# Performance work log

Hardware: AMD Instinct MI355X
Metric: run time of the kernel (lower is better)

## Reference

```python
import jax, jax.numpy as jnp
import numpy as np

N_NODES = 50000
N_EDGES = 800000
IN_DIM = 5
HID = (32, 64, 128, 64, 32)
OUT_DIM = 2
EPS = 1e-5  # nn.BatchNorm1d default eps


def _bn(x, g, b):
    # BatchNorm1d in training mode: batch (biased) statistics over nodes
    m = jnp.mean(x, axis=0)
    v = jnp.var(x, axis=0)
    return (x - m) * jax.lax.rsqrt(v + EPS) * g + b


def setup_inputs() -> dict:
    key = jax.random.key(0)
    ks = jax.random.split(key, 40)
    it = iter(range(40))
    def nrm(shape, s=0.1):
        return jax.random.normal(ks[next(it)], shape, jnp.float32) * s
    inp = {}
    inp["x"] = jax.random.normal(ks[next(it)], (N_NODES, IN_DIM), jnp.float32)
    inp["edge_index"] = jax.random.randint(ks[next(it)], (2, N_EDGES), 0, N_NODES, jnp.int32)
    # input embedding: Linear(5,32) -> ReLU -> BatchNorm1d(32)
    inp["emb_W"] = nrm((IN_DIM, HID[0]))
    inp["emb_b"] = jnp.zeros((HID[0],), jnp.float32)
    inp["emb_g"] = jnp.ones((HID[0],), jnp.float32)
    inp["emb_beta"] = jnp.zeros((HID[0],), jnp.float32)
    # 4 GraphConv blocks
    for i in range(len(HID) - 1):
        din, dout = HID[i], HID[i + 1]
        inp[f"b{i}_Wrel"] = nrm((din, dout))   # lin_rel weight (has bias)
        inp[f"b{i}_brel"] = jnp.zeros((dout,), jnp.float32)
        inp[f"b{i}_Wroot"] = nrm((din, dout))  # lin_root weight (no bias)
        inp[f"b{i}_g"] = jnp.ones((dout,), jnp.float32)
        inp[f"b{i}_beta"] = jnp.zeros((dout,), jnp.float32)
    # output MLP: Linear(32,16) -> ReLU -> Linear(16,2)
    inp["out_W1"] = nrm((HID[-1], HID[-1] // 2))
    inp["out_b1"] = jnp.zeros((HID[-1] // 2,), jnp.float32)
    inp["out_W2"] = nrm((HID[-1] // 2, OUT_DIM))
    inp["out_b2"] = jnp.zeros((OUT_DIM,), jnp.float32)
    return inp


def reference(x, edge_index,
              emb_W, emb_b, emb_g, emb_beta,
              b0_Wrel, b0_brel, b0_Wroot, b0_g, b0_beta,
              b1_Wrel, b1_brel, b1_Wroot, b1_g, b1_beta,
              b2_Wrel, b2_brel, b2_Wroot, b2_g, b2_beta,
              b3_Wrel, b3_brel, b3_Wroot, b3_g, b3_beta,
              out_W1, out_b1, out_W2, out_b2):
    src, dst = edge_index[0], edge_index[1]
    # input embedding: Linear -> ReLU -> BN
    h = jnp.maximum(x @ emb_W + emb_b, 0.0)
    h = _bn(h, emb_g, emb_beta)
    blocks = [
        (b0_Wrel, b0_brel, b0_Wroot, b0_g, b0_beta),
        (b1_Wrel, b1_brel, b1_Wroot, b1_g, b1_beta),
        (b2_Wrel, b2_brel, b2_Wroot, b2_g, b2_beta),
        (b3_Wrel, b3_brel, b3_Wroot, b3_g, b3_beta),
    ]
    for Wrel, brel, Wroot, g, beta in blocks:
        # GraphConv (aggr='add'): lin_rel(sum_{j in N(i)} x_j) + lin_root(x_i)
        agg = jax.ops.segment_sum(h[src], dst, num_segments=N_NODES)
        h = agg @ Wrel + brel + h @ Wroot
        # BN then ReLU (GNNBlock order)
        h = jnp.maximum(_bn(h, g, beta), 0.0)
    # output MLP
    h = jnp.maximum(h @ out_W1 + out_b1, 0.0)
    return h @ out_W2 + out_b2
```

## Files before the change

### kernel.cpp

```cpp
#include <hip/hip_runtime.h>

#define N_NODES 50000
#define N_EDGES 800000
#define BN_EPS 1e-5f

typedef unsigned int   u32;
typedef unsigned short u16;

__device__ __forceinline__ void fma4(float4& a, float s, const float4& w) {
    a.x += s * w.x; a.y += s * w.y; a.z += s * w.z; a.w += s * w.w;
}
__device__ __forceinline__ void add4(float4& a, const float4& b) {
    a.x += b.x; a.y += b.y; a.z += b.z; a.w += b.w;
}
__device__ __forceinline__ u16 f2bf(float f) {
    union { u32 i; float f; } c; c.f = f;
    return (u16)((c.i + 0x7FFFu + ((c.i >> 16) & 1u)) >> 16);
}
__device__ __forceinline__ float4 bf4(uint2 w) {
    union { u32 i; float f; } a, b, c, d;
    a.i = w.x << 16; b.i = w.x & 0xFFFF0000u;
    c.i = w.y << 16; d.i = w.y & 0xFFFF0000u;
    return make_float4(a.f, b.f, c.f, d.f);
}
__device__ __forceinline__ uint2 pack4(const float4& v) {
    uint2 w;
    w.x = (u32)f2bf(v.x) | ((u32)f2bf(v.y) << 16);
    w.y = (u32)f2bf(v.z) | ((u32)f2bf(v.w) << 16);
    return w;
}

template <int NY>
__device__ __forceinline__ bool xcd_decode(int nx, int& x, int& y) {
    const int s = blockIdx.x & (8 * NY - 1);
    const int g = blockIdx.x / (8 * NY);
    x = g * 8 + (s & 7);
    y = s >> 3;
    return x < nx;
}
static inline int xcd_grid(int nx, int ny) { return ((nx + 7) / 8 * 8) * ny; }

__global__ void zero_i(int* __restrict__ p, int n) {
    int i = blockIdx.x * blockDim.x + threadIdx.x;
    int stride = gridDim.x * blockDim.x;
    for (; i < n; i += stride) p[i] = 0;
}

__global__ void hist_kernel(const int* __restrict__ dst, int* __restrict__ cnt) {
    int i = blockIdx.x * blockDim.x + threadIdx.x;
    int stride = gridDim.x * blockDim.x;
    for (; i < N_EDGES; i += stride) atomicAdd(&cnt[dst[i]], 1);
}
__global__ void scan1_kernel(const int* __restrict__ cnt, int* __restrict__ rp,
                             int* __restrict__ bsum) {
    __shared__ int s[256];
    int t = threadIdx.x;
    int idx = blockIdx.x * 256 + t;
    int v = (idx < N_NODES) ? cnt[idx] : 0;
    s[t] = v;
    __syncthreads();
    for (int off = 1; off < 256; off <<= 1) {
        int x = 0;
        if (t >= off) x = s[t - off];
        __syncthreads();
        s[t] += x;
        __syncthreads();
    }
    if (idx < N_NODES) rp[idx] = s[t] - v;
    if (t == 255) bsum[blockIdx.x] = s[255];
}
__global__ void scan2_kernel(int* __restrict__ bsum, int nb, float* __restrict__ stats) {
    __shared__ int s[256];
    int t = threadIdx.x;
    for (int i = t; i < 5 * 256; i += 256) stats[i] = 0.f;
    int v = (t < nb) ? bsum[t] : 0;
    s[t] = v;
    __syncthreads();
    for (int off = 1; off < 256; off <<= 1) {
        int x = 0;
        if (t >= off) x = s[t - off];
        __syncthreads();
        s[t] += x;
        __syncthreads();
    }
    if (t < nb) bsum[t] = s[t] - v;
}
__global__ void scan3_kernel(int* __restrict__ rp, const int* __restrict__ bsum,
                             int* __restrict__ cnt) {
    int idx = blockIdx.x * 256 + threadIdx.x;
    if (idx < N_NODES) {
        rp[idx] += bsum[blockIdx.x];
        cnt[idx] = 0;
    }
    if (idx == 0) rp[N_NODES] = N_EDGES;
}
__global__ void fill_kernel(const int* __restrict__ src, const int* __restrict__ dst,
                            const int* __restrict__ rp, int* __restrict__ cur,
                            u16* __restrict__ ssrc) {
    int i = blockIdx.x * blockDim.x + threadIdx.x;
    int stride = gridDim.x * blockDim.x;
    for (; i < N_EDGES; i += stride) {
        int d = dst[i];
        int p = rp[d] + atomicAdd(&cur[d], 1);
        ssrc[p] = (u16)src[i];
    }
}

__global__ __launch_bounds__(256) void emb_fused(
    const float* __restrict__ x, const float* __restrict__ W,
    const float* __restrict__ b, float* __restrict__ out,
    u16* __restrict__ out16, float* __restrict__ stats) {
    __shared__ float lsum[32], lssq[32];
    if (threadIdx.x < 32) { lsum[threadIdx.x] = 0.f; lssq[threadIdx.x] = 0.f; }
    __syncthreads();
    const int o = threadIdx.x & 31;
    const int total = N_NODES * 32;
    float mys = 0.f, myq = 0.f;
    for (int base = blockIdx.x * 256; base < total; base += gridDim.x * 256) {
        int idx = base + threadIdx.x;
        float acc = 0.f;
        if (idx < total) {
            int n = idx >> 5;
            const float* xr = x + n * 5;
            acc = b[o];
#pragma unroll
            for (int k = 0; k < 5; ++k) acc += xr[k] * W[k * 32 + o];
            acc = fmaxf(acc, 0.f);
            out[idx] = acc;
            out16[idx] = f2bf(acc);
        }
        mys += acc;
        myq += acc * acc;
    }
    mys += __shfl_xor(mys, 32);
    myq += __shfl_xor(myq, 32);
    if ((threadIdx.x & 63) < 32) { atomicAdd(&lsum[o], mys); atomicAdd(&lssq[o], myq); }
    __syncthreads();
    if (threadIdx.x < 32) {
        atomicAdd(&stats[threadIdx.x], lsum[threadIdx.x]);
        atomicAdd(&stats[32 + threadIdx.x], lssq[threadIdx.x]);
    }
}

template <int D>
__device__ __forceinline__ void bn_finalize_lds(
    const float* __restrict__ stats, const float* __restrict__ g,
    const float* __restrict__ beta, float* sc, float* sh) {
    const float invN = 1.f / (float)N_NODES;
    for (int f = threadIdx.x; f < D; f += 256) {
        float m = stats[f] * invN;
        float var = stats[D + f] * invN - m * m;
        float a = g[f] * rsqrtf(var + BN_EPS);
        sc[f] = a;
        sh[f] = beta[f] - m * a;
    }
    __syncthreads();
}

__global__ __launch_bounds__(256) void bn_apply16(
    float4* __restrict__ h, u16* __restrict__ out16,
    const float* __restrict__ g, const float* __restrict__ beta,
    const float* __restrict__ stats, int logD) {
    const int D = 1 << logD;
    const int total4 = N_NODES << (logD - 2);
    const float invN = 1.f / (float)N_NODES;
    int idx = blockIdx.x * blockDim.x + threadIdx.x;
    int stride = gridDim.x * blockDim.x;
    for (; idx < total4; idx += stride) {
        int f = (idx & ((D >> 2) - 1)) << 2;
        float4 v = h[idx];
        float* vp = (float*)&v;
#pragma unroll
        for (int c = 0; c < 4; ++c) {
            float m = stats[f + c] * invN;
            float var = stats[D + f + c] * invN - m * m;
            vp[c] = fmaxf((vp[c] - m) * rsqrtf(var + BN_EPS) * g[f + c] + beta[f + c], 0.f);
        }
        h[idx] = v;
        ((uint2*)out16)[idx] = pack4(v);
    }
}

template <int LOGD>
__global__ __launch_bounds__(256) void gather_agg_bf16(
    const u16* __restrict__ h16, const int* __restrict__ rp,
    const u16* __restrict__ ssrc, float4* __restrict__ agg) {
    constexpr int QSH = LOGD - 2;
    int tid = blockIdx.x * 256 + threadIdx.x;
    int node = tid >> QSH;
    if (node >= N_NODES) return;
    int q = tid & ((1 << QSH) - 1);
    int e0 = rp[node], e1 = rp[node + 1];
    float4 acc = make_float4(0.f, 0.f, 0.f, 0.f);
    int e = e0;
    for (; e + 4 <= e1; e += 4) {
        int s0 = ssrc[e], s1 = ssrc[e + 1], s2 = ssrc[e + 2], s3 = ssrc[e + 3];
        uint2 w0 = ((const uint2*)(h16 + ((size_t)s0 << LOGD)))[q];
        uint2 w1 = ((const uint2*)(h16 + ((size_t)s1 << LOGD)))[q];
        uint2 w2 = ((const uint2*)(h16 + ((size_t)s2 << LOGD)))[q];
        uint2 w3 = ((const uint2*)(h16 + ((size_t)s3 << LOGD)))[q];
        float4 v0 = bf4(w0), v1 = bf4(w1), v2 = bf4(w2), v3 = bf4(w3);
        add4(v0, v1); add4(v2, v3); add4(acc, v0); add4(acc, v2);
    }
    for (; e < e1; ++e) {
        float4 v = bf4(((const uint2*)(h16 + ((size_t)ssrc[e] << LOGD)))[q]);
        add4(acc, v);
    }
    agg[tid] = acc;
}

template <int DIN, int DOUT, int OBL>
__global__ __launch_bounds__(256) void gconv_bn0(
    const float* __restrict__ h, const float* __restrict__ agg,
    const float* __restrict__ Wrel, const float* __restrict__ brel,
    const float* __restrict__ Wroot, float* __restrict__ out,
    const float* __restrict__ stats_in, const float* __restrict__ g_in,
    const float* __restrict__ beta_in, const int* __restrict__ deg,
    float* __restrict__ stats_out, int nx) {
    constexpr int NY = 2;
    constexpr int LPN = OBL / 4;
    constexpr int SLOTS = 256 / LPN;
    constexpr int NPT = 4;
    constexpr int KS = 8;
    constexpr int TOT4 = DIN * OBL / 4;
    int bx, by;
    if (!xcd_decode<NY>(nx, bx, by)) return;
    __shared__ __align__(16) float wl[2 * DIN * OBL];
    __shared__ __align__(16) float sc[DIN];
    __shared__ __align__(16) float sh[DIN];
    __shared__ float lsum[OBL], lssq[OBL];
    const int ob0 = by * OBL;
    for (int e4 = threadIdx.x; e4 < TOT4; e4 += 256) {
        int k = e4 / (OBL / 4);
        int j = (e4 % (OBL / 4)) * 4;
        ((float4*)wl)[e4] = *(const float4*)(Wrel + (size_t)k * DOUT + ob0 + j);
        ((float4*)wl)[TOT4 + e4] = *(const float4*)(Wroot + (size_t)k * DOUT + ob0 + j);
    }
    if (threadIdx.x < OBL) { lsum[threadIdx.x] = 0.f; lssq[threadIdx.x] = 0.f; }
    bn_finalize_lds<DIN>(stats_in, g_in, beta_in, sc, sh);

    const int q = threadIdx.x & (LPN - 1);
    const int slot = threadIdx.x / LPN;
    const int o0 = ob0 + q * 4;
    const int nbase = bx * (SLOTS * NPT) + slot;

    float degf[NPT];
#pragma unroll
    for (int i = 0; i < NPT; ++i) {
        int n = nbase + i * SLOTS;
        degf[i] = (n < N_NODES) ? (float)deg[n] : 0.f;
    }

    float4 bias = *(const float4*)(brel + o0);
    float4 acc[NPT];
#pragma unroll
    for (int i = 0; i < NPT; ++i) acc[i] = bias;

#pragma unroll 1
    for (int s = 0; s < DIN / KS; ++s) {
        const int k0 = s * KS;
        float4 s2[2] = {((const float4*)sc)[k0 / 4], ((const float4*)sc)[k0 / 4 + 1]};
        float4 t2[2] = {((const float4*)sh)[k0 / 4], ((const float4*)sh)[k0 / 4 + 1]};
        const float* scp = (const float*)s2;
        const float* shp = (const float*)t2;
        float4 hv[NPT][2], av[NPT][2];
#pragma unroll
        for (int i = 0; i < NPT; ++i) {
            int n = nbase + i * SLOTS;
            int nn = (n < N_NODES) ? n : 0;
            const float4* hr = (const float4*)(h + (size_t)nn * DIN + k0);
            const float4* ar = (const float4*)(agg + (size_t)nn * DIN + k0);
            hv[i][0] = hr[0]; hv[i][1] = hr[1];
            av[i][0] = ar[0]; av[i][1] = ar[1];
        }
#pragma unroll
        for (int kk = 0; kk < KS; ++kk) {
            float4 wr = *(const float4*)&wl[(k0 + kk) * OBL + q * 4];
            float4 wo = *(const float4*)&wl[DIN * OBL + (k0 + kk) * OBL + q * 4];
#pragma unroll
            for (int i = 0; i < NPT; ++i) {
                float a  = fmaf(((const float*)av[i])[kk], scp[kk], degf[i] * shp[kk]);
                float hh = fmaf(((const float*)hv[i])[kk], scp[kk], shp[kk]);
                fma4(acc[i], a, wr);
                fma4(acc[i], hh, wo);
            }
        }
    }
#pragma unroll
    for (int i = 0; i < NPT; ++i) {
        int n = nbase + i * SLOTS;
        if (n < N_NODES)
            *(float4*)(out + (size_t)n * DOUT + o0) = acc[i];
        else
            acc[i] = make_float4(0.f, 0.f, 0.f, 0.f);
    }
    float4 s4 = make_float4(0.f, 0.f, 0.f, 0.f);
    float4 q4 = make_float4(0.f, 0.f, 0.f, 0.f);
#pragma unroll
    for (int i = 0; i < NPT; ++i) {
        s4.x += acc[i].x; s4.y += acc[i].y; s4.z += acc[i].z; s4.w += acc[i].w;
        q4.x += acc[i].x * acc[i].x; q4.y += acc[i].y * acc[i].y;
        q4.z += acc[i].z * acc[i].z; q4.w += acc[i].w * acc[i].w;
    }
#pragma unroll
    for (int d = LPN; d < 64; d <<= 1) {
        s4.x += __shfl_xor(s4.x, d); s4.y += __shfl_xor(s4.y, d);
        s4.z += __shfl_xor(s4.z, d); s4.w += __shfl_xor(s4.w, d);
        q4.x += __shfl_xor(q4.x, d); q4.y += __shfl_xor(q4.y, d);
        q4.z += __shfl_xor(q4.z, d); q4.w += __shfl_xor(q4.w, d);
    }
    if ((threadIdx.x & 63) < LPN) {
        int c = q * 4;
        atomicAdd(&lsum[c + 0], s4.x); atomicAdd(&lsum[c + 1], s4.y);
        atomicAdd(&lsum[c + 2], s4.z); atomicAdd(&lsum[c + 3], s4.w);
        atomicAdd(&lssq[c + 0], q4.x); atomicAdd(&lssq[c + 1], q4.y);
        atomicAdd(&lssq[c + 2], q4.z); atomicAdd(&lssq[c + 3], q4.w);
    }
    __syncthreads();
    if (threadIdx.x < OBL) {
        atomicAdd(&stats_out[ob0 + threadIdx.x], lsum[threadIdx.x]);
        atomicAdd(&stats_out[DOUT + ob0 + threadIdx.x], lssq[threadIdx.x]);
    }
}

template <int DIN, int DOUT, int OBL>
__global__ __launch_bounds__(256) void gconv_lds(
    const float* __restrict__ h, const float* __restrict__ agg,
    const float* __restrict__ Wrel, const float* __restrict__ brel,
    const float* __restrict__ Wroot, float* __restrict__ out,
    float* __restrict__ stats_out, int nx) {
    constexpr int NY = DOUT / OBL;
    constexpr int LPN = OBL / 4;
    constexpr int SLOTS = 256 / LPN;
    constexpr int NPT = 4;
    constexpr int KS = 8;
    constexpr int TOT4 = DIN * OBL / 4;
    int bx, by;
    if (!xcd_decode<NY>(nx, bx, by)) return;
    __shared__ __align__(16) float wl[2 * DIN * OBL];
    __shared__ float lsum[OBL], lssq[OBL];
    const int ob0 = by * OBL;
    for (int e4 = threadIdx.x; e4 < TOT4; e4 += 256) {
        int k = e4 / (OBL / 4);
        int j = (e4 % (OBL / 4)) * 4;
        ((float4*)wl)[e4] = *(const float4*)(Wrel + (size_t)k * DOUT + ob0 + j);
        ((float4*)wl)[TOT4 + e4] = *(const float4*)(Wroot + (size_t)k * DOUT + ob0 + j);
    }
    if (threadIdx.x < OBL) { lsum[threadIdx.x] = 0.f; lssq[threadIdx.x] = 0.f; }
    __syncthreads();

    const int q = threadIdx.x & (LPN - 1);
    const int slot = threadIdx.x / LPN;
    const int o0 = ob0 + q * 4;
    const int nbase = bx * (SLOTS * NPT) + slot;

    float4 bias = *(const float4*)(brel + o0);
    float4 acc[NPT];
#pragma unroll
    for (int i = 0; i < NPT; ++i) acc[i] = bias;

#pragma unroll 1
    for (int s = 0; s < DIN / KS; ++s) {
        const int k0 = s * KS;
        float4 hv[NPT][2], av[NPT][2];
#pragma unroll
        for (int i = 0; i < NPT; ++i) {
            int n = nbase + i * SLOTS;
            int nn = (n < N_NODES) ? n : 0;
            const float4* hr = (const float4*)(h + (size_t)nn * DIN + k0);
            const float4* ar = (const float4*)(agg + (size_t)nn * DIN + k0);
            hv[i][0] = hr[0]; hv[i][1] = hr[1];
            av[i][0] = ar[0]; av[i][1] = ar[1];
        }
#pragma unroll
        for (int kk = 0; kk < KS; ++kk) {
            float4 wr = *(const float4*)&wl[(k0 + kk) * OBL + q * 4];
            float4 wo = *(const float4*)&wl[DIN * OBL + (k0 + kk) * OBL + q * 4];
#pragma unroll
            for (int i = 0; i < NPT; ++i) {
                fma4(acc[i], ((const float*)av[i])[kk], wr);
                fma4(acc[i], ((const float*)hv[i])[kk], wo);
            }
        }
    }
#pragma unroll
    for (int i = 0; i < NPT; ++i) {
        int n = nbase + i * SLOTS;
        if (n < N_NODES)
            *(float4*)(out + (size_t)n * DOUT + o0) = acc[i];
        else
            acc[i] = make_float4(0.f, 0.f, 0.f, 0.f);
    }
    float4 s4 = make_float4(0.f, 0.f, 0.f, 0.f);
    float4 q4 = make_float4(0.f, 0.f, 0.f, 0.f);
#pragma unroll
    for (int i = 0; i < NPT; ++i) {
        s4.x += acc[i].x; s4.y += acc[i].y; s4.z += acc[i].z; s4.w += acc[i].w;
        q4.x += acc[i].x * acc[i].x; q4.y += acc[i].y * acc[i].y;
        q4.z += acc[i].z * acc[i].z; q4.w += acc[i].w * acc[i].w;
    }
#pragma unroll
    for (int d = LPN; d < 64; d <<= 1) {
        s4.x += __shfl_xor(s4.x, d); s4.y += __shfl_xor(s4.y, d);
        s4.z += __shfl_xor(s4.z, d); s4.w += __shfl_xor(s4.w, d);
        q4.x += __shfl_xor(q4.x, d); q4.y += __shfl_xor(q4.y, d);
        q4.z += __shfl_xor(q4.z, d); q4.w += __shfl_xor(q4.w, d);
    }
    if ((threadIdx.x & 63) < LPN) {
        int c = q * 4;
        atomicAdd(&lsum[c + 0], s4.x); atomicAdd(&lsum[c + 1], s4.y);
        atomicAdd(&lsum[c + 2], s4.z); atomicAdd(&lsum[c + 3], s4.w);
        atomicAdd(&lssq[c + 0], q4.x); atomicAdd(&lssq[c + 1], q4.y);
        atomicAdd(&lssq[c + 2], q4.z); atomicAdd(&lssq[c + 3], q4.w);
    }
    __syncthreads();
    if (threadIdx.x < OBL) {
        atomicAdd(&stats_out[ob0 + threadIdx.x], lsum[threadIdx.x]);
        atomicAdd(&stats_out[DOUT + ob0 + threadIdx.x], lssq[threadIdx.x]);
    }
}

template <int DIN, int DOUT, int OBL>
__global__ __launch_bounds__(256) void prem_bn(
    const float* __restrict__ h, const float* __restrict__ Wrel,
    const float* __restrict__ brel, const float* __restrict__ Wroot,
    u16* __restrict__ P16, float* __restrict__ Q,
    const float* __restrict__ stats_in, const float* __restrict__ g_in,
    const float* __restrict__ beta_in, int nx) {
    constexpr int NY = DOUT / OBL;
    constexpr int LPN = OBL / 4;
    constexpr int SLOTS = 256 / LPN;
    constexpr int NPT = 4;
    constexpr int KS = 8;
    constexpr int TOT4 = DIN * OBL / 4;
    int bx, by;
    if (!xcd_decode<NY>(nx, bx, by)) return;
    __shared__ __align__(16) float wl[2 * DIN * OBL];
    __shared__ __align__(16) float sc[DIN];
    __shared__ __align__(16) float sh[DIN];
    const int ob0 = by * OBL;
    for (int e4 = threadIdx.x; e4 < TOT4; e4 += 256) {
        int k = e4 / (OBL / 4);
        int j = (e4 % (OBL / 4)) * 4;
        ((float4*)wl)[e4] = *(const float4*)(Wrel + (size_t)k * DOUT + ob0 + j);
        ((float4*)wl)[TOT4 + e4] = *(const float4*)(Wroot + (size_t)k * DOUT + ob0 + j);
    }
    bn_finalize_lds<DIN>(stats_in, g_in, beta_in, sc, sh);

    const int q = threadIdx.x & (LPN - 1);
    const int slot = threadIdx.x / LPN;
    const int o0 = ob0 + q * 4;
    const int nbase = bx * (SLOTS * NPT) + slot;

    float4 bias = *(const float4*)(brel + o0);
    float4 accp[NPT], accq[NPT];
#pragma unroll
    for (int i = 0; i < NPT; ++i) {
        accp[i] = make_float4(0.f, 0.f, 0.f, 0.f);
        accq[i] = bias;
    }

#pragma unroll 1
    for (int s = 0; s < DIN / KS; ++s) {
        const int k0 = s * KS;
        float4 s2[2] = {((const float4*)sc)[k0 / 4], ((const float4*)sc)[k0 / 4 + 1]};
        float4 t2[2] = {((const float4*)sh)[k0 / 4], ((const float4*)sh)[k0 / 4 + 1]};
        const float* scp = (const float*)s2;
        const float* shp = (const float*)t2;
        float4 hv[NPT][2];
#pragma unroll
        for (int i = 0; i < NPT; ++i) {
            int n = nbase + i * SLOTS;
            int nn = (n < N_NODES) ? n : 0;
            const float4* hr = (const float4*)(h + (size_t)nn * DIN + k0);
            hv[i][0] = hr[0]; hv[i][1] = hr[1];
        }
#pragma unroll
        for (int kk = 0; kk < KS; ++kk) {
            float4 wr = *(const float4*)&wl[(k0 + kk) * OBL + q * 4];
            float4 wo = *(const float4*)&wl[DIN * OBL + (k0 + kk) * OBL + q * 4];
#pragma unroll
            for (int i = 0; i < NPT; ++i) {
                float hh = fmaxf(fmaf(((const float*)hv[i])[kk], scp[kk], shp[kk]), 0.f);
                fma4(accp[i], hh, wr);
                fma4(accq[i], hh, wo);
            }
        }
    }
#pragma unroll
    for (int i = 0; i < NPT; ++i) {
        int n = nbase + i * SLOTS;
        if (n < N_NODES) {
            *(uint2*)(P16 + (size_t)n * DOUT + o0) = pack4(accp[i]);
            *(float4*)(Q + (size_t)n * DOUT + o0) = accq[i];
        }
    }
}

template <int LOGD>
__global__ __launch_bounds__(256) void gather_add_bf16(
    const u16* __restrict__ P16, const int* __restrict__ rp,
    const u16* __restrict__ ssrc, float4* __restrict__ out,
    float* __restrict__ stats) {
    constexpr int D = 1 << LOGD;
    constexpr int Q4 = D / 4;
    __shared__ float lsum[D], lssq[D];
    if (threadIdx.x < D) { lsum[threadIdx.x] = 0.f; lssq[threadIdx.x] = 0.f; }
    __syncthreads();

    const int total = N_NODES * Q4;
    const int q = threadIdx.x & (Q4 - 1);
    float4 mys = make_float4(0.f, 0.f, 0.f, 0.f);
    float4 myq = make_float4(0.f, 0.f, 0.f, 0.f);

    for (int base = blockIdx.x * 256; base < total; base += gridDim.x * 256) {
        int tid = base + threadIdx.x;
        float4 acc = make_float4(0.f, 0.f, 0.f, 0.f);
        if (tid < total) {
            int node = tid >> (LOGD - 2);
            int e0 = rp[node], e1 = rp[node + 1];
            acc = out[tid];
            int e = e0;
            for (; e + 4 <= e1; e += 4) {
                int s0 = ssrc[e], s1 = ssrc[e + 1], s2 = ssrc[e + 2], s3 = ssrc[e + 3];
                uint2 w0 = ((const uint2*)(P16 + ((size_t)s0 << LOGD)))[q];
                uint2 w1 = ((const uint2*)(P16 + ((size_t)s1 << LOGD)))[q];
                uint2 w2 = ((const uint2*)(P16 + ((size_t)s2 << LOGD)))[q];
                uint2 w3 = ((const uint2*)(P16 + ((size_t)s3 << LOGD)))[q];
                float4 v0 = bf4(w0), v1 = bf4(w1), v2 = bf4(w2), v3 = bf4(w3);
                add4(v0, v1); add4(v2, v3); add4(acc, v0); add4(acc, v2);
            }
            for (; e < e1; ++e) {
                float4 v = bf4(((const uint2*)(P16 + ((size_t)ssrc[e] << LOGD)))[q]);
                add4(acc, v);
            }
            out[tid] = acc;
        }
        mys.x += acc.x; mys.y += acc.y; mys.z += acc.z; mys.w += acc.w;
        myq.x += acc.x * acc.x; myq.y += acc.y * acc.y;
        myq.z += acc.z * acc.z; myq.w += acc.w * acc.w;
    }
#pragma unroll
    for (int d = Q4; d < 64; d <<= 1) {
        mys.x += __shfl_xor(mys.x, d); mys.y += __shfl_xor(mys.y, d);
        mys.z += __shfl_xor(mys.z, d); mys.w += __shfl_xor(mys.w, d);
        myq.x += __shfl_xor(myq.x, d); myq.y += __shfl_xor(myq.y, d);
        myq.z += __shfl_xor(myq.z, d); myq.w += __shfl_xor(myq.w, d);
    }
    if ((threadIdx.x & 63) < Q4) {
        atomicAdd(&lsum[4 * q + 0], mys.x); atomicAdd(&lsum[4 * q + 1], mys.y);
        atomicAdd(&lsum[4 * q + 2], mys.z); atomicAdd(&lsum[4 * q + 3], mys.w);
        atomicAdd(&lssq[4 * q + 0], myq.x); atomicAdd(&lssq[4 * q + 1], myq.y);
        atomicAdd(&lssq[4 * q + 2], myq.z); atomicAdd(&lssq[4 * q + 3], myq.w);
    }
    __syncthreads();
    if (threadIdx.x < D) {
        atomicAdd(&stats[threadIdx.x], lsum[threadIdx.x]);
        atomicAdd(&stats[D + threadIdx.x], lssq[threadIdx.x]);
    }
}

__global__ __launch_bounds__(256) void outmlp_kernel(
    const float* __restrict__ h, const float* __restrict__ stats,
    const float* __restrict__ g, const float* __restrict__ beta,
    const float* __restrict__ W1, const float* __restrict__ b1,
    const float* __restrict__ W2, const float* __restrict__ b2,
    float* __restrict__ out) {
    int n = blockIdx.x * 256 + threadIdx.x;
    if (n >= N_NODES) return;
    const float invN = 1.f / (float)N_NODES;
    const float4* hr4 = (const float4*)(h + (size_t)n * 32);
    float hv[32];
#pragma unroll
    for (int k4 = 0; k4 < 8; ++k4) {
        float4 v = hr4[k4];
        float* vp = (float*)&v;
#pragma unroll
        for (int c = 0; c < 4; ++c) {
            int f = 4 * k4 + c;
            float m = stats[f] * invN;
            float var = stats[32 + f] * invN - m * m;
            hv[f] = fmaxf((vp[c] - m) * rsqrtf(var + BN_EPS) * g[f] + beta[f], 0.f);
        }
    }
    float hid[16];
#pragma unroll
    for (int j = 0; j < 16; ++j) hid[j] = b1[j];
#pragma unroll
    for (int k = 0; k < 32; ++k) {
        float hk = hv[k];
#pragma unroll
        for (int j = 0; j < 16; ++j) hid[j] += hk * W1[k * 16 + j];
    }
    float o0 = b2[0], o1 = b2[1];
#pragma unroll
    for (int j = 0; j < 16; ++j) {
        float t = fmaxf(hid[j], 0.f);
        o0 += t * W2[j * 2 + 0];
        o1 += t * W2[j * 2 + 1];
    }
    out[n * 2 + 0] = o0;
    out[n * 2 + 1] = o1;
}

extern "C" void kernel_launch(void* const* d_in, const int* in_sizes, int n_in,
                              void* d_out, int out_size, void* d_ws, size_t ws_size,
                              hipStream_t stream) {
    const float* x        = (const float*)d_in[0];
    const int*   ei       = (const int*)d_in[1];
    const int*   src      = ei;
    const int*   dst      = ei + N_EDGES;
    const float* emb_W    = (const float*)d_in[2];
    const float* emb_b    = (const float*)d_in[3];
    const float* emb_g    = (const float*)d_in[4];
    const float* emb_beta = (const float*)d_in[5];
    const float* out_W1   = (const float*)d_in[26];
    const float* out_b1   = (const float*)d_in[27];
    const float* out_W2   = (const float*)d_in[28];
    const float* out_b2   = (const float*)d_in[29];

    float* ws = (float*)d_ws;
    const size_t HMAX = (size_t)N_NODES * 128;
    float* hA    = ws;
    float* hB    = ws + HMAX;
    float* AGG   = ws + 2 * HMAX;
    u16*   P16   = (u16*)AGG;
    float* stats = AGG + (size_t)N_NODES * 64;
    u16*   h16   = (u16*)(stats + 5 * 256);
    int*   rp    = (int*)(h16 + (size_t)N_NODES * 64);
    int*   cnt   = rp + N_NODES + 1;
    int*   bsum  = cnt + N_NODES;
    u16*   ssrc  = (u16*)(bsum + 256);

    float* st0 = stats;
    float* st1 = stats + 256;
    float* st2 = stats + 512;
    float* st3 = stats + 768;
    float* st4 = stats + 1024;

    const int BS = 256;
    const int NB = (N_NODES + BS - 1) / BS;

    zero_i<<<64, BS, 0, stream>>>(cnt, N_NODES);
    hist_kernel<<<1024, BS, 0, stream>>>(dst, cnt);
    scan1_kernel<<<NB, 256, 0, stream>>>(cnt, rp, bsum);
    scan2_kernel<<<1, 256, 0, stream>>>(bsum, NB, stats);
    scan3_kernel<<<NB, 256, 0, stream>>>(rp, bsum, cnt);
    fill_kernel<<<1024, BS, 0, stream>>>(src, dst, rp, cnt, ssrc);

    emb_fused<<<512, BS, 0, stream>>>(x, emb_W, emb_b, hA, h16, st0);

    gather_agg_bf16<5><<<(N_NODES * 8 + BS - 1) / BS, BS, 0, stream>>>(h16, rp, ssrc, (float4*)AGG);
    {
        const int nx = (N_NODES + 127) / 128;
        gconv_bn0<32, 64, 32><<<xcd_grid(nx, 2), BS, 0, stream>>>(
            hA, AGG, (const float*)d_in[6], (const float*)d_in[7], (const float*)d_in[8], hB,
            st0, emb_g, emb_beta, cnt, st1, nx);
    }
    bn_apply16<<<2048, BS, 0, stream>>>((float4*)hB, h16, (const float*)d_in[9], (const float*)d_in[10], st1, 6);

    gather_agg_bf16<6><<<(N_NODES * 16 + BS - 1) / BS, BS, 0, stream>>>(h16, rp, ssrc, (float4*)AGG);
    {
        const int nx = (N_NODES + 127) / 128;
        gconv_lds<64, 128, 32><<<xcd_grid(nx, 4), BS, 0, stream>>>(
            hB, AGG, (const float*)d_in[11], (const float*)d_in[12], (const float*)d_in[13], hA, st2, nx);
    }

    {
        const int nx = (N_NODES + 255) / 256;
        prem_bn<128, 64, 16><<<xcd_grid(nx, 4), BS, 0, stream>>>(
            hA, (const float*)d_in[16], (const float*)d_in[17], (const float*)d_in[18], P16, hB,
            st2, (const float*)d_in[14], (const float*)d_in[15], nx);
    }
    gather_add_bf16<6><<<512, BS, 0, stream>>>(P16, rp, ssrc, (float4*)hB, st3);

    {
        const int nx = (N_NODES + 255) / 256;
        prem_bn<64, 32, 16><<<xcd_grid(nx, 2), BS, 0, stream>>>(
            hB, (const float*)d_in[21], (const float*)d_in[22], (const float*)d_in[23], P16, hA,
            st3, (const float*)d_in[19], (const float*)d_in[20], nx);
    }
    gather_add_bf16<5><<<512, BS, 0, stream>>>(P16, rp, ssrc, (float4*)hA, st4);

    outmlp_kernel<<<NB, BS, 0, stream>>>(
        hA, st4, (const float*)d_in[24], (const float*)d_in[25],
        out_W1, out_b1, out_W2, out_b2, (float*)d_out);
}
```

Measured before the change: 360.2 us.

## Store aggregates and hidden inputs in bf16 for the first two GraphConv layers

The gather kernels now write the neighbour aggregate as packed bf16 instead of fp32, and the first two GraphConv matmul kernels read both the aggregate and the hidden state from bf16 buffers. The fp32 hidden-state writes in the embedding and BN-apply kernels are dropped. This cuts global memory traffic for writing and re-reading the aggregate and hidden tensors. The cost is extra rounding of the aggregate and root inputs, which can reduce accuracy, and a small amount of unpacking ALU work in the inner loop.

```diff
diff --git a/kernel.cpp b/kernel.cpp
--- a/kernel.cpp
+++ b/kernel.cpp
@@ -28,6 +28,12 @@
     w.x = (u32)f2bf(v.x) | ((u32)f2bf(v.y) << 16);
     w.y = (u32)f2bf(v.z) | ((u32)f2bf(v.w) << 16);
     return w;
+}
+__device__ __forceinline__ float bfx(const uint4& v, int kk) {
+    u32 w = ((const u32*)&v)[kk >> 1];
+    union { u32 i; float f; } c;
+    c.i = (kk & 1) ? (w & 0xFFFF0000u) : (w << 16);
+    return c.f;
 }
 
 template <int NY>
@@ -108,8 +114,8 @@
 
 __global__ __launch_bounds__(256) void emb_fused(
     const float* __restrict__ x, const float* __restrict__ W,
-    const float* __restrict__ b, float* __restrict__ out,
-    u16* __restrict__ out16, float* __restrict__ stats) {
+    const float* __restrict__ b, u16* __restrict__ out16,
+    float* __restrict__ stats) {
     __shared__ float lsum[32], lssq[32];
     if (threadIdx.x < 32) { lsum[threadIdx.x] = 0.f; lssq[threadIdx.x] = 0.f; }
     __syncthreads();
@@ -126,7 +132,6 @@
 #pragma unroll
             for (int k = 0; k < 5; ++k) acc += xr[k] * W[k * 32 + o];
             acc = fmaxf(acc, 0.f);
-            out[idx] = acc;
             out16[idx] = f2bf(acc);
         }
         mys += acc;
@@ -158,7 +163,7 @@
 }
 
 __global__ __launch_bounds__(256) void bn_apply16(
-    float4* __restrict__ h, u16* __restrict__ out16,
+    const float4* __restrict__ h, u16* __restrict__ out16,
     const float* __restrict__ g, const float* __restrict__ beta,
     const float* __restrict__ stats, int logD) {
     const int D = 1 << logD;
@@ -176,7 +181,6 @@
             float var = stats[D + f + c] * invN - m * m;
             vp[c] = fmaxf((vp[c] - m) * rsqrtf(var + BN_EPS) * g[f + c] + beta[f + c], 0.f);
         }
-        h[idx] = v;
         ((uint2*)out16)[idx] = pack4(v);
     }
 }
@@ -184,7 +188,7 @@
 template <int LOGD>
 __global__ __launch_bounds__(256) void gather_agg_bf16(
     const u16* __restrict__ h16, const int* __restrict__ rp,
-    const u16* __restrict__ ssrc, float4* __restrict__ agg) {
+    const u16* __restrict__ ssrc, uint2* __restrict__ agg16) {
     constexpr int QSH = LOGD - 2;
     int tid = blockIdx.x * 256 + threadIdx.x;
     int node = tid >> QSH;
@@ -206,12 +210,12 @@
         float4 v = bf4(((const uint2*)(h16 + ((size_t)ssrc[e] << LOGD)))[q]);
         add4(acc, v);
     }
-    agg[tid] = acc;
+    agg16[tid] = pack4(acc);
 }
 
 template <int DIN, int DOUT, int OBL>
 __global__ __launch_bounds__(256) void gconv_bn0(
-    const float* __restrict__ h, const float* __restrict__ agg,
+    const u16* __restrict__ h16, const u16* __restrict__ agg16,
     const float* __restrict__ Wrel, const float* __restrict__ brel,
     const float* __restrict__ Wroot, float* __restrict__ out,
     const float* __restrict__ stats_in, const float* __restrict__ g_in,
@@ -263,15 +267,13 @@
         float4 t2[2] = {((const float4*)sh)[k0 / 4], ((const float4*)sh)[k0 / 4 + 1]};
         const float* scp = (const float*)s2;
         const float* shp = (const float*)t2;
-        float4 hv[NPT][2], av[NPT][2];
+        uint4 hv16[NPT], av16[NPT];
 #pragma unroll
         for (int i = 0; i < NPT; ++i) {
             int n = nbase + i * SLOTS;
             int nn = (n < N_NODES) ? n : 0;
-            const float4* hr = (const float4*)(h + (size_t)nn * DIN + k0);
-            const float4* ar = (const float4*)(agg + (size_t)nn * DIN + k0);
-            hv[i][0] = hr[0]; hv[i][1] = hr[1];
-            av[i][0] = ar[0]; av[i][1] = ar[1];
+            hv16[i] = *(const uint4*)(h16 + (size_t)nn * DIN + k0);
+            av16[i] = *(const uint4*)(agg16 + (size_t)nn * DIN + k0);
         }
 #pragma unroll
         for (int kk = 0; kk < KS; ++kk) {
@@ -279,8 +281,8 @@
             float4 wo = *(const float4*)&wl[DIN * OBL + (k0 + kk) * OBL + q * 4];
 #pragma unroll
             for (int i = 0; i < NPT; ++i) {
-                float a  = fmaf(((const float*)av[i])[kk], scp[kk], degf[i] * shp[kk]);
-                float hh = fmaf(((const float*)hv[i])[kk], scp[kk], shp[kk]);
+                float a  = fmaf(bfx(av16[i], kk), scp[kk], degf[i] * shp[kk]);
+                float hh = fmaf(bfx(hv16[i], kk), scp[kk], shp[kk]);
                 fma4(acc[i], a, wr);
                 fma4(acc[i], hh, wo);
             }
@@ -325,7 +327,7 @@
 
 template <int DIN, int DOUT, int OBL>
 __global__ __launch_bounds__(256) void gconv_lds(
-    const float* __restrict__ h, const float* __restrict__ agg,
+    const u16* __restrict__ h16, const u16* __restrict__ agg16,
     const float* __restrict__ Wrel, const float* __restrict__ brel,
     const float* __restrict__ Wroot, float* __restrict__ out,
     float* __restrict__ stats_out, int nx) {
@@ -362,15 +364,13 @@
 #pragma unroll 1
     for (int s = 0; s < DIN / KS; ++s) {
         const int k0 = s * KS;
-        float4 hv[NPT][2], av[NPT][2];
+        uint4 hv16[NPT], av16[NPT];
 #pragma unroll
         for (int i = 0; i < NPT; ++i) {
             int n = nbase + i * SLOTS;
             int nn = (n < N_NODES) ? n : 0;
-            const float4* hr = (const float4*)(h + (size_t)nn * DIN + k0);
-            const float4* ar = (const float4*)(agg + (size_t)nn * DIN + k0);
-            hv[i][0] = hr[0]; hv[i][1] = hr[1];
-            av[i][0] = ar[0]; av[i][1] = ar[1];
+            hv16[i] = *(const uint4*)(h16 + (size_t)nn * DIN + k0);
+            av16[i] = *(const uint4*)(agg16 + (size_t)nn * DIN + k0);
         }
 #pragma unroll
         for (int kk = 0; kk < KS; ++kk) {
@@ -378,8 +378,8 @@
             float4 wo = *(const float4*)&wl[DIN * OBL + (k0 + kk) * OBL + q * 4];
 #pragma unroll
             for (int i = 0; i < NPT; ++i) {
-                fma4(acc[i], ((const float*)av[i])[kk], wr);
-                fma4(acc[i], ((const float*)hv[i])[kk], wo);
+                fma4(acc[i], bfx(av16[i], kk), wr);
+                fma4(acc[i], bfx(hv16[i], kk), wo);
             }
         }
     }
@@ -623,9 +623,9 @@
     const size_t HMAX = (size_t)N_NODES * 128;
     float* hA    = ws;
     float* hB    = ws + HMAX;
-    float* AGG   = ws + 2 * HMAX;
-    u16*   P16   = (u16*)AGG;
-    float* stats = AGG + (size_t)N_NODES * 64;
+    u16*   AGG16 = (u16*)(ws + 2 * HMAX);
+    u16*   P16   = AGG16;
+    float* stats = ws + 2 * HMAX + (size_t)N_NODES * 32;
     u16*   h16   = (u16*)(stats + 5 * 256);
     int*   rp    = (int*)(h16 + (size_t)N_NODES * 64);
     int*   cnt   = rp + N_NODES + 1;
@@ -648,22 +648,22 @@
     scan3_kernel<<<NB, 256, 0, stream>>>(rp, bsum, cnt);
     fill_kernel<<<1024, BS, 0, stream>>>(src, dst, rp, cnt, ssrc);
 
-    emb_fused<<<512, BS, 0, stream>>>(x, emb_W, emb_b, hA, h16, st0);
-
-    gather_agg_bf16<5><<<(N_NODES * 8 + BS - 1) / BS, BS, 0, stream>>>(h16, rp, ssrc, (float4*)AGG);
+    emb_fused<<<512, BS, 0, stream>>>(x, emb_W, emb_b, h16, st0);
+
+    gather_agg_bf16<5><<<(N_NODES * 8 + BS - 1) / BS, BS, 0, stream>>>(h16, rp, ssrc, (uint2*)AGG16);
     {
         const int nx = (N_NODES + 127) / 128;
         gconv_bn0<32, 64, 32><<<xcd_grid(nx, 2), BS, 0, stream>>>(
-            hA, AGG, (const float*)d_in[6], (const float*)d_in[7], (const float*)d_in[8], hB,
+            h16, AGG16, (const float*)d_in[6], (const float*)d_in[7], (const float*)d_in[8], hB,
             st0, emb_g, emb_beta, cnt, st1, nx);
     }
-    bn_apply16<<<2048, BS, 0, stream>>>((float4*)hB, h16, (const float*)d_in[9], (const float*)d_in[10], st1, 6);
-
-    gather_agg_bf16<6><<<(N_NODES * 16 + BS - 1) / BS, BS, 0, stream>>>(h16, rp, ssrc, (float4*)AGG);
+    bn_apply16<<<2048, BS, 0, stream>>>((const float4*)hB, h16, (const float*)d_in[9], (const float*)d_in[10], st1, 6);
+
+    gather_agg_bf16<6><<<(N_NODES * 16 + BS - 1) / BS, BS, 0, stream>>>(h16, rp, ssrc, (uint2*)AGG16);
     {
         const int nx = (N_NODES + 127) / 128;
         gconv_lds<64, 128, 32><<<xcd_grid(nx, 4), BS, 0, stream>>>(
-            hB, AGG, (const float*)d_in[11], (const float*)d_in[12], (const float*)d_in[13], hA, st2, nx);
+            h16, AGG16, (const float*)d_in[11], (const float*)d_in[12], (const float*)d_in[13], hA, st2, nx);
     }
 
     {
```

Measured after the change: 349.6 us. 1.03x faster.
